# Kernel optimization log

Hardware: AMD Instinct MI355X
Metric: run time of the kernel (lower is better)

## Reference

```python
import jax, jax.numpy as jnp
import numpy as np

N_NODES = 50000
N_EDGES = 800000
N_FEAT = 128
N_HIDDEN = 128
N_CLASSES = 64


def sage_mean_conv(x, src, dst, W_self, W_neigh, b, n_nodes):
    # DGL SAGEConv (mean): out = x @ W_self + mean_neigh(x) @ W_neigh + b
    # mean over in-neighbors: messages flow src -> dst
    msg = x[src]  # [E, F] gather
    h_sum = jax.ops.segment_sum(msg, dst, num_segments=n_nodes)  # [N, F]
    deg = jax.ops.segment_sum(jnp.ones((src.shape[0],), x.dtype), dst,
                              num_segments=n_nodes)
    h_mean = h_sum / jnp.maximum(deg, 1.0)[:, None]
    return x @ W_self + h_mean @ W_neigh + b


def setup_inputs() -> dict:
    key = jax.random.key(0)
    ks = jax.random.split(key, 8)
    sc1 = 1.0 / np.sqrt(N_FEAT)
    sc2 = 1.0 / np.sqrt(N_HIDDEN)
    return {
        "x": jax.random.normal(ks[0], (N_NODES, N_FEAT), jnp.float32),
        "W_self1": jax.random.normal(ks[1], (N_FEAT, N_HIDDEN), jnp.float32) * sc1,
        "W_neigh1": jax.random.normal(ks[2], (N_FEAT, N_HIDDEN), jnp.float32) * sc1,
        "b1": jnp.zeros((N_HIDDEN,), jnp.float32),
        "W_self2": jax.random.normal(ks[3], (N_HIDDEN, N_CLASSES), jnp.float32) * sc2,
        "W_neigh2": jax.random.normal(ks[4], (N_HIDDEN, N_CLASSES), jnp.float32) * sc2,
        "b2": jnp.zeros((N_CLASSES,), jnp.float32),
        "src": jax.random.randint(ks[5], (N_EDGES,), 0, N_NODES, jnp.int32),
        "dst": jax.random.randint(ks[6], (N_EDGES,), 0, N_NODES, jnp.int32),
    }


def reference(x, W_self1, W_neigh1, b1, W_self2, W_neigh2, b2, src, dst):
    n = x.shape[0]
    h = sage_mean_conv(x, src, dst, W_self1, W_neigh1, b1, n)
    h = jax.nn.relu(h)
    logits = sage_mean_conv(h, src, dst, W_self2, W_neigh2, b2, n)
    return logits
```

## Files before the change

### kernel.cpp

```cpp
#include <hip/hip_runtime.h>

#define N_NODES 50000
#define N_EDGES 800000
#define N_FEAT 128
#define N_HIDDEN 128
#define N_CLASSES 64

#define NBUCK 256
#define BUCK_NODES 196
#define BIN_CHUNK 8192
#define BIN_BLK ((N_EDGES + BIN_CHUNK - 1) / BIN_CHUNK)

#define CAST_BLK 6250
#define PACK1_BLK 16
#define PACK2_BLK 8
#define PREP_BLK (CAST_BLK + BIN_BLK + PACK1_BLK + PACK2_BLK)
#define GEMM1_BLK ((N_NODES + 31) / 32)
#define BG_BLK (BIN_BLK + GEMM1_BLK)

typedef __attribute__((ext_vector_type(8))) short bf16x8;
typedef __attribute__((ext_vector_type(4))) float f32x4;

__device__ __forceinline__ unsigned short f32_to_bf16(float f) {
    unsigned int u = __float_as_uint(f);
    return (unsigned short)((u + 0x7fffu + ((u >> 16) & 1u)) >> 16);
}
__device__ __forceinline__ float bf16lo(unsigned int v) { return __uint_as_float(v << 16); }
__device__ __forceinline__ float bf16hi(unsigned int v) { return __uint_as_float(v & 0xffff0000u); }

template <int NOUT>
__device__ void pack_w_body(int idx, const float* __restrict__ Wself,
                            const float* __restrict__ Wneigh,
                            unsigned short* __restrict__ Bp) {
    constexpr int NT = NOUT / 16;
    constexpr int NO = NOUT / 2;
    if (idx >= 4 * NT * 64) return;
    const int lane = idx & 63;
    const int tc = idx >> 6;
    const int c = tc % NT;
    const int t = tc / NT;
    const int n = c * 16 + (lane & 15);
    const int k0 = t * 32 + (lane >> 4) * 8;
    const float* W = (n < NO) ? Wself : Wneigh;
    const int nn = (n < NO) ? n : n - NO;
    ushort4 lo, hi;
    lo.x = f32_to_bf16(W[(k0 + 0) * NO + nn]);
    lo.y = f32_to_bf16(W[(k0 + 1) * NO + nn]);
    lo.z = f32_to_bf16(W[(k0 + 2) * NO + nn]);
    lo.w = f32_to_bf16(W[(k0 + 3) * NO + nn]);
    hi.x = f32_to_bf16(W[(k0 + 4) * NO + nn]);
    hi.y = f32_to_bf16(W[(k0 + 5) * NO + nn]);
    hi.z = f32_to_bf16(W[(k0 + 6) * NO + nn]);
    hi.w = f32_to_bf16(W[(k0 + 7) * NO + nn]);
    ((ushort4*)&Bp[(size_t)idx * 8])[0] = lo;
    ((ushort4*)&Bp[(size_t)idx * 8])[1] = hi;
}

__device__ void a0_body(int blk, const int* __restrict__ dst, int* __restrict__ bcount) {
    __shared__ int h[NBUCK];
    const int t = threadIdx.x;
    h[t] = 0;
    __syncthreads();
    const int lo = blk * BIN_CHUNK;
    const int hi = min(lo + BIN_CHUNK, N_EDGES);
    for (int i = lo + t; i < hi; i += 256) {
        atomicAdd(&h[dst[i] / BUCK_NODES], 1);
    }
    __syncthreads();
    if (h[t] > 0) atomicAdd(&bcount[t], h[t]);
}

__global__ __launch_bounds__(256) void prep_kernel(
        const float* __restrict__ x, unsigned short* __restrict__ xb,
        const int* __restrict__ dst, int* __restrict__ bcount,
        const float* __restrict__ Ws1, const float* __restrict__ Wn1,
        unsigned short* __restrict__ Bp1,
        const float* __restrict__ Ws2, const float* __restrict__ Wn2,
        unsigned short* __restrict__ Bp2) {
    const int b = blockIdx.x;
    const int t = threadIdx.x;
    if (b < CAST_BLK) {
        int i = b * 256 + t;
        float4 v = ((const float4*)x)[i];
        ushort4 o;
        o.x = f32_to_bf16(v.x);
        o.y = f32_to_bf16(v.y);
        o.z = f32_to_bf16(v.z);
        o.w = f32_to_bf16(v.w);
        ((ushort4*)xb)[i] = o;
    } else if (b < CAST_BLK + BIN_BLK) {
        a0_body(b - CAST_BLK, dst, bcount);
    } else if (b < CAST_BLK + BIN_BLK + PACK1_BLK) {
        int idx = (b - CAST_BLK - BIN_BLK) * 256 + t;
        pack_w_body<256>(idx, Ws1, Wn1, Bp1);
    } else {
        int idx = (b - CAST_BLK - BIN_BLK - PACK1_BLK) * 256 + t;
        pack_w_body<128>(idx, Ws2, Wn2, Bp2);
    }
}

__global__ __launch_bounds__(256) void bscan_kernel(const int* __restrict__ bcount,
                                                    int* __restrict__ bstart,
                                                    int* __restrict__ bcursor) {
    __shared__ int sc[NBUCK];
    const int t = threadIdx.x;
    const int v = bcount[t];
    sc[t] = v;
    __syncthreads();
    for (int s = 1; s < NBUCK; s <<= 1) {
        int u = (t >= s) ? sc[t - s] : 0;
        __syncthreads();
        sc[t] += u;
        __syncthreads();
    }
    const int excl = sc[t] - v;
    bstart[t] = excl;
    bcursor[t] = excl;
    if (t == NBUCK - 1) bstart[NBUCK] = sc[t];
}

__device__ void a1_body(int blk, const int* __restrict__ src, const int* __restrict__ dst,
                        int* __restrict__ bcursor, unsigned int* __restrict__ binned) {
    __shared__ int h[NBUCK];
    __shared__ int base[NBUCK];
    const int t = threadIdx.x;
    h[t] = 0;
    __syncthreads();
    const int lo = blk * BIN_CHUNK;
    const int hi = min(lo + BIN_CHUNK, N_EDGES);
    for (int i = lo + t; i < hi; i += 256) {
        atomicAdd(&h[dst[i] / BUCK_NODES], 1);
    }
    __syncthreads();
    if (h[t] > 0) base[t] = atomicAdd(&bcursor[t], h[t]);
    h[t] = 0;
    __syncthreads();
    for (int i = lo + t; i < hi; i += 256) {
        const int d = dst[i];
        const int b = d / BUCK_NODES;
        const int r = atomicAdd(&h[b], 1);
        binned[base[b] + r] = ((unsigned int)(d - b * BUCK_NODES) << 16) | (unsigned int)src[i];
    }
}

template <int NOUT>
__device__ void gemm_mfma_body(int gblk,
                               const unsigned short* __restrict__ xb,
                               const unsigned short* __restrict__ Bp,
                               const float* __restrict__ bias,
                               float* __restrict__ s,
                               unsigned short* __restrict__ p) {
    constexpr int NT = NOUT / 16;
    constexpr int NO = NOUT / 2;
    constexpr int NSUB = NT / 4;

    const int tid = threadIdx.x;
    const int wave = tid >> 6;
    const int lane = tid & 63;
    const int mcol = lane & 15;
    const int kgrp = lane >> 4;

    const int mbase = gblk * 32;
    int r0 = mbase + mcol;       if (r0 >= N_NODES) r0 = N_NODES - 1;
    int r1 = mbase + 16 + mcol;  if (r1 >= N_NODES) r1 = N_NODES - 1;

    f32x4 acc[2][NSUB];
#pragma unroll
    for (int mt = 0; mt < 2; ++mt)
#pragma unroll
        for (int c = 0; c < NSUB; ++c)
            acc[mt][c] = (f32x4){0.f, 0.f, 0.f, 0.f};

#pragma unroll
    for (int t = 0; t < 4; ++t) {
        bf16x8 a0 = *(const bf16x8*)&xb[(size_t)r0 * 128 + t * 32 + kgrp * 8];
        bf16x8 a1 = *(const bf16x8*)&xb[(size_t)r1 * 128 + t * 32 + kgrp * 8];
#pragma unroll
        for (int c = 0; c < NSUB; ++c) {
            const int ct = wave * NSUB + c;
            bf16x8 bfrag = *(const bf16x8*)&Bp[((size_t)(t * NT + ct) * 64 + lane) * 8];
            acc[0][c] = __builtin_amdgcn_mfma_f32_16x16x32_bf16(a0, bfrag, acc[0][c], 0, 0, 0);
            acc[1][c] = __builtin_amdgcn_mfma_f32_16x16x32_bf16(a1, bfrag, acc[1][c], 0, 0, 0);
        }
    }

    float bv[NSUB];
    int ncols[NSUB];
#pragma unroll
    for (int c = 0; c < NSUB; ++c) {
        ncols[c] = (wave * NSUB + c) * 16 + mcol;
        bv[c] = (ncols[c] < NO) ? bias[ncols[c]] : 0.f;
    }

#pragma unroll
    for (int mt = 0; mt < 2; ++mt) {
#pragma unroll
        for (int c = 0; c < NSUB; ++c) {
            const int ncol = ncols[c];
#pragma unroll
            for (int r = 0; r < 4; ++r) {
                const int node = mbase + mt * 16 + kgrp * 4 + r;
                if (node >= N_NODES) continue;
                const float v = acc[mt][c][r];
                if (ncol < NO) {
                    s[(size_t)node * NO + ncol] = v + bv[c];
                } else {
                    p[(size_t)node * NO + (ncol - NO)] = f32_to_bf16(v);
                }
            }
        }
    }
}

__global__ __launch_bounds__(256) void bin_gemm1_kernel(
        const int* __restrict__ src, const int* __restrict__ dst,
        int* __restrict__ bcursor, unsigned int* __restrict__ binned,
        const unsigned short* __restrict__ xb,
        const unsigned short* __restrict__ Bp1,
        const float* __restrict__ b1,
        float* __restrict__ s1, unsigned short* __restrict__ p1) {
    const int b = blockIdx.x;
    if (b < BIN_BLK) {
        a1_body(b, src, dst, bcursor, binned);
    } else {
        gemm_mfma_body<256>(b - BIN_BLK, xb, Bp1, b1, s1, p1);
    }
}

__global__ __launch_bounds__(256) void bucket_build_kernel(
        const unsigned int* __restrict__ binned,
        const int* __restrict__ bstart,
        int* __restrict__ offsets,
        unsigned short* __restrict__ csr16) {
    __shared__ int cnt[NBUCK];
    __shared__ int pre[NBUCK];
    const int b = blockIdx.x;
    const int t = threadIdx.x;
    const int n0 = b * BUCK_NODES;
    const int nn = min(N_NODES - n0, BUCK_NODES);
    const int e0 = bstart[b];
    const int e1 = bstart[b + 1];

    cnt[t] = 0;
    __syncthreads();
    for (int i = e0 + t; i < e1; i += 256) {
        atomicAdd(&cnt[binned[i] >> 16], 1);
    }
    __syncthreads();
    int v = cnt[t];
    pre[t] = v;
    __syncthreads();
    for (int s = 1; s < NBUCK; s <<= 1) {
        int u = (t >= s) ? pre[t - s] : 0;
        __syncthreads();
        pre[t] += u;
        __syncthreads();
    }
    const int excl = pre[t] - v;
    if (t < nn) offsets[n0 + t] = e0 + excl;
    if (b == 0 && t == 0) offsets[N_NODES] = N_EDGES;
    __syncthreads();
    pre[t] = excl;
    cnt[t] = 0;
    __syncthreads();
    for (int i = e0 + t; i < e1; i += 256) {
        const unsigned int u = binned[i];
        const int dl = (int)(u >> 16);
        const int r = atomicAdd(&cnt[dl], 1);
        csr16[e0 + pre[dl] + r] = (unsigned short)(u & 0xffffu);
    }
}

__global__ __launch_bounds__(256) void gemm2_kernel(
        const unsigned short* __restrict__ h1b,
        const unsigned short* __restrict__ Bp2,
        const float* __restrict__ b2,
        float* __restrict__ s2, unsigned short* __restrict__ p2) {
    gemm_mfma_body<128>(blockIdx.x, h1b, Bp2, b2, s2, p2);
}

__global__ __launch_bounds__(256) void agg_relu_128_kernel(
        const float* __restrict__ s,
        const unsigned short* __restrict__ p,
        const int* __restrict__ offsets,
        const unsigned short* __restrict__ csr16,
        unsigned short* __restrict__ h1b) {
    const int wave = threadIdx.x >> 6;
    const int lane = threadIdx.x & 63;
    const int half = lane >> 5;
    const int l = lane & 31;
    const int node = blockIdx.x * 4 + wave;
    if (node >= N_NODES) return;

    const int off0 = offsets[node];
    const int off1 = offsets[node + 1];
    const uint2* pp = (const uint2*)p;

    float a0 = 0.f, a1 = 0.f, a2 = 0.f, a3 = 0.f;
    int i = off0 + half;
    for (; i + 14 < off1; i += 16) {
        uint2 v0 = pp[(size_t)csr16[i + 0] * 32 + l];
        uint2 v1 = pp[(size_t)csr16[i + 2] * 32 + l];
        uint2 v2 = pp[(size_t)csr16[i + 4] * 32 + l];
        uint2 v3 = pp[(size_t)csr16[i + 6] * 32 + l];
        uint2 v4 = pp[(size_t)csr16[i + 8] * 32 + l];
        uint2 v5 = pp[(size_t)csr16[i + 10] * 32 + l];
        uint2 v6 = pp[(size_t)csr16[i + 12] * 32 + l];
        uint2 v7 = pp[(size_t)csr16[i + 14] * 32 + l];
        a0 += bf16lo(v0.x) + bf16lo(v1.x) + bf16lo(v2.x) + bf16lo(v3.x)
            + bf16lo(v4.x) + bf16lo(v5.x) + bf16lo(v6.x) + bf16lo(v7.x);
        a1 += bf16hi(v0.x) + bf16hi(v1.x) + bf16hi(v2.x) + bf16hi(v3.x)
            + bf16hi(v4.x) + bf16hi(v5.x) + bf16hi(v6.x) + bf16hi(v7.x);
        a2 += bf16lo(v0.y) + bf16lo(v1.y) + bf16lo(v2.y) + bf16lo(v3.y)
            + bf16lo(v4.y) + bf16lo(v5.y) + bf16lo(v6.y) + bf16lo(v7.y);
        a3 += bf16hi(v0.y) + bf16hi(v1.y) + bf16hi(v2.y) + bf16hi(v3.y)
            + bf16hi(v4.y) + bf16hi(v5.y) + bf16hi(v6.y) + bf16hi(v7.y);
    }
    for (; i < off1; i += 2) {
        uint2 v = pp[(size_t)csr16[i] * 32 + l];
        a0 += bf16lo(v.x);
        a1 += bf16hi(v.x);
        a2 += bf16lo(v.y);
        a3 += bf16hi(v.y);
    }
    a0 += __shfl_xor(a0, 32);
    a1 += __shfl_xor(a1, 32);
    a2 += __shfl_xor(a2, 32);
    a3 += __shfl_xor(a3, 32);

    if (half == 0) {
        const float invdeg = 1.0f / fmaxf((float)(off1 - off0), 1.0f);
        float4 sv = ((const float4*)s)[(size_t)node * 32 + l];
        ushort4 o;
        o.x = f32_to_bf16(fmaxf(sv.x + a0 * invdeg, 0.f));
        o.y = f32_to_bf16(fmaxf(sv.y + a1 * invdeg, 0.f));
        o.z = f32_to_bf16(fmaxf(sv.z + a2 * invdeg, 0.f));
        o.w = f32_to_bf16(fmaxf(sv.w + a3 * invdeg, 0.f));
        ((ushort4*)h1b)[(size_t)node * 32 + l] = o;
    }
}

__global__ __launch_bounds__(256) void agg_64_kernel(
        const unsigned short* __restrict__ p,
        const int* __restrict__ offsets,
        const unsigned short* __restrict__ csr16,
        float* __restrict__ out) {
    const int wave = threadIdx.x >> 6;
    const int lane = threadIdx.x & 63;
    const int q = lane >> 4;
    const int l = lane & 15;
    const int node = blockIdx.x * 4 + wave;
    if (node >= N_NODES) return;

    const int off0 = offsets[node];
    const int off1 = offsets[node + 1];
    const uint2* pp = (const uint2*)p;

    float a0 = 0.f, a1 = 0.f, a2 = 0.f, a3 = 0.f;
    int i = off0 + q;
    for (; i + 12 < off1; i += 16) {
        uint2 v0 = pp[(size_t)csr16[i + 0] * 16 + l];
        uint2 v1 = pp[(size_t)csr16[i + 4] * 16 + l];
        uint2 v2 = pp[(size_t)csr16[i + 8] * 16 + l];
        uint2 v3 = pp[(size_t)csr16[i + 12] * 16 + l];
        a0 += bf16lo(v0.x) + bf16lo(v1.x) + bf16lo(v2.x) + bf16lo(v3.x);
        a1 += bf16hi(v0.x) + bf16hi(v1.x) + bf16hi(v2.x) + bf16hi(v3.x);
        a2 += bf16lo(v0.y) + bf16lo(v1.y) + bf16lo(v2.y) + bf16lo(v3.y);
        a3 += bf16hi(v0.y) + bf16hi(v1.y) + bf16hi(v2.y) + bf16hi(v3.y);
    }
    for (; i < off1; i += 4) {
        uint2 v = pp[(size_t)csr16[i] * 16 + l];
        a0 += bf16lo(v.x);
        a1 += bf16hi(v.x);
        a2 += bf16lo(v.y);
        a3 += bf16hi(v.y);
    }
    a0 += __shfl_xor(a0, 16); a0 += __shfl_xor(a0, 32);
    a1 += __shfl_xor(a1, 16); a1 += __shfl_xor(a1, 32);
    a2 += __shfl_xor(a2, 16); a2 += __shfl_xor(a2, 32);
    a3 += __shfl_xor(a3, 16); a3 += __shfl_xor(a3, 32);

    if (q == 0) {
        const float invdeg = 1.0f / fmaxf((float)(off1 - off0), 1.0f);
        float4 sv = ((float4*)out)[(size_t)node * 16 + l];
        sv.x += a0 * invdeg;
        sv.y += a1 * invdeg;
        sv.z += a2 * invdeg;
        sv.w += a3 * invdeg;
        ((float4*)out)[(size_t)node * 16 + l] = sv;
    }
}

extern "C" void kernel_launch(void* const* d_in, const int* in_sizes, int n_in,
                              void* d_out, int out_size, void* d_ws, size_t ws_size,
                              hipStream_t stream) {
    const float* x        = (const float*)d_in[0];
    const float* W_self1  = (const float*)d_in[1];
    const float* W_neigh1 = (const float*)d_in[2];
    const float* b1       = (const float*)d_in[3];
    const float* W_self2  = (const float*)d_in[4];
    const float* W_neigh2 = (const float*)d_in[5];
    const float* b2       = (const float*)d_in[6];
    const int*   src      = (const int*)d_in[7];
    const int*   dst      = (const int*)d_in[8];
    float* out = (float*)d_out;

    int* bcount  = (int*)d_ws;
    int* bstart  = bcount + 256;
    int* bcursor = bstart + 288;
    int* offsets = bcursor + 256;
    unsigned int* binned = (unsigned int*)(offsets + 50048);
    unsigned short* csr16 = (unsigned short*)(binned + 800000);
    unsigned short* Bp1 = csr16 + 800000;
    unsigned short* Bp2 = Bp1 + 32768;
    unsigned short* xb  = Bp2 + 16384;
    unsigned short* h1b = xb;
    float* s1 = (float*)(xb + (size_t)N_NODES * 128);
    unsigned short* p1 = (unsigned short*)(s1 + (size_t)N_NODES * 128);
    unsigned short* p2 = p1;

    hipMemsetAsync(bcount, 0, 256 * sizeof(int), stream);
    prep_kernel<<<PREP_BLK, 256, 0, stream>>>(x, xb, dst, bcount,
                                              W_self1, W_neigh1, Bp1,
                                              W_self2, W_neigh2, Bp2);

    bscan_kernel<<<1, 256, 0, stream>>>(bcount, bstart, bcursor);

    bin_gemm1_kernel<<<BG_BLK, 256, 0, stream>>>(src, dst, bcursor, binned,
                                                 xb, Bp1, b1, s1, p1);

    bucket_build_kernel<<<NBUCK, 256, 0, stream>>>(binned, bstart, offsets, csr16);

    agg_relu_128_kernel<<<(N_NODES + 3) / 4, 256, 0, stream>>>(s1, p1, offsets, csr16, h1b);

    gemm2_kernel<<<(N_NODES + 31) / 32, 256, 0, stream>>>(h1b, Bp2, b2, out, p2);
    agg_64_kernel<<<(N_NODES + 3) / 4, 256, 0, stream>>>(p2, offsets, csr16, out);
}
```

Before: 232.0 us.

## Store layer-1 neighbor projections in FP8, reuse per-chunk histograms, widen gather loads

Layer-1 neighbor projections are now stored as FP8 instead of bf16, which halves the bytes moved by the random gather in the first aggregation. Both aggregation kernels are restructured to issue 8 or 4 independent masked wide gathers per iteration, giving more loads in flight. The binning pass now stores per-chunk histograms, so the second pass reuses them instead of recounting, and the memset and global bucket-count atomics are dropped. FP8 storage loses precision in the layer-1 neighbor term and may exceed the accuracy tolerance.

```diff
diff --git a/kernel.cpp b/kernel.cpp
--- a/kernel.cpp
+++ b/kernel.cpp
@@ -1,4 +1,5 @@
 #include <hip/hip_runtime.h>
+#include <hip/hip_fp16.h>
 
 #define N_NODES 50000
 #define N_EDGES 800000
@@ -8,7 +9,7 @@
 
 #define NBUCK 256
 #define BUCK_NODES 196
-#define BIN_CHUNK 8192
+#define BIN_CHUNK 2048
 #define BIN_BLK ((N_EDGES + BIN_CHUNK - 1) / BIN_CHUNK)
 
 #define CAST_BLK 6250
@@ -20,6 +21,7 @@
 
 typedef __attribute__((ext_vector_type(8))) short bf16x8;
 typedef __attribute__((ext_vector_type(4))) float f32x4;
+typedef __attribute__((ext_vector_type(2))) float f32x2;
 
 __device__ __forceinline__ unsigned short f32_to_bf16(float f) {
     unsigned int u = __float_as_uint(f);
@@ -27,6 +29,34 @@
 }
 __device__ __forceinline__ float bf16lo(unsigned int v) { return __uint_as_float(v << 16); }
 __device__ __forceinline__ float bf16hi(unsigned int v) { return __uint_as_float(v & 0xffff0000u); }
+
+#if defined(__has_builtin)
+#if __has_builtin(__builtin_amdgcn_cvt_pk_f32_fp8) && __has_builtin(__builtin_amdgcn_cvt_pk_fp8_f32)
+#define FP8_HW 1
+#endif
+#endif
+
+__device__ __forceinline__ unsigned char f32_to_fp8(float f) {
+#ifdef FP8_HW
+    return (unsigned char)(__builtin_amdgcn_cvt_pk_fp8_f32(f, f, 0, false) & 0xff);
+#else
+    unsigned short hb = __half_as_ushort(__float2half(f));
+    return (unsigned char)((hb + 0x7fu + ((hb >> 8) & 1u)) >> 8);
+#endif
+}
+
+__device__ __forceinline__ void fp8x4_to_f32(unsigned int u, float* o) {
+#ifdef FP8_HW
+    f32x2 lo = __builtin_amdgcn_cvt_pk_f32_fp8(u, false);
+    f32x2 hi = __builtin_amdgcn_cvt_pk_f32_fp8(u, true);
+    o[0] = lo.x; o[1] = lo.y; o[2] = hi.x; o[3] = hi.y;
+#else
+    o[0] = __half2float(__ushort_as_half((unsigned short)((u & 0xffu) << 8)));
+    o[1] = __half2float(__ushort_as_half((unsigned short)(((u >> 8) & 0xffu) << 8)));
+    o[2] = __half2float(__ushort_as_half((unsigned short)(((u >> 16) & 0xffu) << 8)));
+    o[3] = __half2float(__ushort_as_half((unsigned short)(((u >> 24) & 0xffu) << 8)));
+#endif
+}
 
 template <int NOUT>
 __device__ void pack_w_body(int idx, const float* __restrict__ Wself,
@@ -56,7 +86,7 @@
     ((ushort4*)&Bp[(size_t)idx * 8])[1] = hi;
 }
 
-__device__ void a0_body(int blk, const int* __restrict__ dst, int* __restrict__ bcount) {
+__device__ void a0_body(int blk, const int* __restrict__ dst, int* __restrict__ hists) {
     __shared__ int h[NBUCK];
     const int t = threadIdx.x;
     h[t] = 0;
@@ -67,12 +97,12 @@
         atomicAdd(&h[dst[i] / BUCK_NODES], 1);
     }
     __syncthreads();
-    if (h[t] > 0) atomicAdd(&bcount[t], h[t]);
+    hists[blk * NBUCK + t] = h[t];
 }
 
 __global__ __launch_bounds__(256) void prep_kernel(
         const float* __restrict__ x, unsigned short* __restrict__ xb,
-        const int* __restrict__ dst, int* __restrict__ bcount,
+        const int* __restrict__ dst, int* __restrict__ hists,
         const float* __restrict__ Ws1, const float* __restrict__ Wn1,
         unsigned short* __restrict__ Bp1,
         const float* __restrict__ Ws2, const float* __restrict__ Wn2,
@@ -89,7 +119,7 @@
         o.w = f32_to_bf16(v.w);
         ((ushort4*)xb)[i] = o;
     } else if (b < CAST_BLK + BIN_BLK) {
-        a0_body(b - CAST_BLK, dst, bcount);
+        a0_body(b - CAST_BLK, dst, hists);
     } else if (b < CAST_BLK + BIN_BLK + PACK1_BLK) {
         int idx = (b - CAST_BLK - BIN_BLK) * 256 + t;
         pack_w_body<256>(idx, Ws1, Wn1, Bp1);
@@ -99,12 +129,14 @@
     }
 }
 
-__global__ __launch_bounds__(256) void bscan_kernel(const int* __restrict__ bcount,
+__global__ __launch_bounds__(256) void bscan_kernel(const int* __restrict__ hists,
                                                     int* __restrict__ bstart,
                                                     int* __restrict__ bcursor) {
     __shared__ int sc[NBUCK];
     const int t = threadIdx.x;
-    const int v = bcount[t];
+    int v = 0;
+#pragma unroll 8
+    for (int c = 0; c < BIN_BLK; ++c) v += hists[c * NBUCK + t];
     sc[t] = v;
     __syncthreads();
     for (int s = 1; s < NBUCK; s <<= 1) {
@@ -120,36 +152,33 @@
 }
 
 __device__ void a1_body(int blk, const int* __restrict__ src, const int* __restrict__ dst,
+                        const int* __restrict__ hists,
                         int* __restrict__ bcursor, unsigned int* __restrict__ binned) {
-    __shared__ int h[NBUCK];
     __shared__ int base[NBUCK];
+    __shared__ int cnt[NBUCK];
     const int t = threadIdx.x;
-    h[t] = 0;
+    const int h = hists[blk * NBUCK + t];
+    base[t] = atomicAdd(&bcursor[t], h);
+    cnt[t] = 0;
     __syncthreads();
     const int lo = blk * BIN_CHUNK;
     const int hi = min(lo + BIN_CHUNK, N_EDGES);
     for (int i = lo + t; i < hi; i += 256) {
-        atomicAdd(&h[dst[i] / BUCK_NODES], 1);
-    }
-    __syncthreads();
-    if (h[t] > 0) base[t] = atomicAdd(&bcursor[t], h[t]);
-    h[t] = 0;
-    __syncthreads();
-    for (int i = lo + t; i < hi; i += 256) {
         const int d = dst[i];
         const int b = d / BUCK_NODES;
-        const int r = atomicAdd(&h[b], 1);
+        const int r = atomicAdd(&cnt[b], 1);
         binned[base[b] + r] = ((unsigned int)(d - b * BUCK_NODES) << 16) | (unsigned int)src[i];
     }
 }
 
-template <int NOUT>
+template <int NOUT, bool PFP8>
 __device__ void gemm_mfma_body(int gblk,
                                const unsigned short* __restrict__ xb,
                                const unsigned short* __restrict__ Bp,
                                const float* __restrict__ bias,
                                float* __restrict__ s,
-                               unsigned short* __restrict__ p) {
+                               unsigned char* __restrict__ p8,
+                               unsigned short* __restrict__ p16) {
     constexpr int NT = NOUT / 16;
     constexpr int NO = NOUT / 2;
     constexpr int NSUB = NT / 4;
@@ -204,8 +233,10 @@
                 const float v = acc[mt][c][r];
                 if (ncol < NO) {
                     s[(size_t)node * NO + ncol] = v + bv[c];
+                } else if (PFP8) {
+                    p8[(size_t)node * NO + (ncol - NO)] = f32_to_fp8(v);
                 } else {
-                    p[(size_t)node * NO + (ncol - NO)] = f32_to_bf16(v);
+                    p16[(size_t)node * NO + (ncol - NO)] = f32_to_bf16(v);
                 }
             }
         }
@@ -214,16 +245,17 @@
 
 __global__ __launch_bounds__(256) void bin_gemm1_kernel(
         const int* __restrict__ src, const int* __restrict__ dst,
+        const int* __restrict__ hists,
         int* __restrict__ bcursor, unsigned int* __restrict__ binned,
         const unsigned short* __restrict__ xb,
         const unsigned short* __restrict__ Bp1,
         const float* __restrict__ b1,
-        float* __restrict__ s1, unsigned short* __restrict__ p1) {
+        float* __restrict__ s1, unsigned char* __restrict__ p1) {
     const int b = blockIdx.x;
     if (b < BIN_BLK) {
-        a1_body(b, src, dst, bcursor, binned);
+        a1_body(b, src, dst, hists, bcursor, binned);
     } else {
-        gemm_mfma_body<256>(b - BIN_BLK, xb, Bp1, b1, s1, p1);
+        gemm_mfma_body<256, true>(b - BIN_BLK, xb, Bp1, b1, s1, p1, nullptr);
     }
 }
 
@@ -276,19 +308,19 @@
         const unsigned short* __restrict__ Bp2,
         const float* __restrict__ b2,
         float* __restrict__ s2, unsigned short* __restrict__ p2) {
-    gemm_mfma_body<128>(blockIdx.x, h1b, Bp2, b2, s2, p2);
+    gemm_mfma_body<128, false>(blockIdx.x, h1b, Bp2, b2, s2, nullptr, p2);
 }
 
 __global__ __launch_bounds__(256) void agg_relu_128_kernel(
         const float* __restrict__ s,
-        const unsigned short* __restrict__ p,
+        const unsigned char* __restrict__ p,
         const int* __restrict__ offsets,
         const unsigned short* __restrict__ csr16,
         unsigned short* __restrict__ h1b) {
     const int wave = threadIdx.x >> 6;
     const int lane = threadIdx.x & 63;
-    const int half = lane >> 5;
-    const int l = lane & 31;
+    const int q = lane >> 4;
+    const int l = lane & 15;
     const int node = blockIdx.x * 4 + wave;
     if (node >= N_NODES) return;
 
@@ -296,47 +328,55 @@
     const int off1 = offsets[node + 1];
     const uint2* pp = (const uint2*)p;
 
-    float a0 = 0.f, a1 = 0.f, a2 = 0.f, a3 = 0.f;
-    int i = off0 + half;
-    for (; i + 14 < off1; i += 16) {
-        uint2 v0 = pp[(size_t)csr16[i + 0] * 32 + l];
-        uint2 v1 = pp[(size_t)csr16[i + 2] * 32 + l];
-        uint2 v2 = pp[(size_t)csr16[i + 4] * 32 + l];
-        uint2 v3 = pp[(size_t)csr16[i + 6] * 32 + l];
-        uint2 v4 = pp[(size_t)csr16[i + 8] * 32 + l];
-        uint2 v5 = pp[(size_t)csr16[i + 10] * 32 + l];
-        uint2 v6 = pp[(size_t)csr16[i + 12] * 32 + l];
-        uint2 v7 = pp[(size_t)csr16[i + 14] * 32 + l];
-        a0 += bf16lo(v0.x) + bf16lo(v1.x) + bf16lo(v2.x) + bf16lo(v3.x)
-            + bf16lo(v4.x) + bf16lo(v5.x) + bf16lo(v6.x) + bf16lo(v7.x);
-        a1 += bf16hi(v0.x) + bf16hi(v1.x) + bf16hi(v2.x) + bf16hi(v3.x)
-            + bf16hi(v4.x) + bf16hi(v5.x) + bf16hi(v6.x) + bf16hi(v7.x);
-        a2 += bf16lo(v0.y) + bf16lo(v1.y) + bf16lo(v2.y) + bf16lo(v3.y)
-            + bf16lo(v4.y) + bf16lo(v5.y) + bf16lo(v6.y) + bf16lo(v7.y);
-        a3 += bf16hi(v0.y) + bf16hi(v1.y) + bf16hi(v2.y) + bf16hi(v3.y)
-            + bf16hi(v4.y) + bf16hi(v5.y) + bf16hi(v6.y) + bf16hi(v7.y);
-    }
-    for (; i < off1; i += 2) {
-        uint2 v = pp[(size_t)csr16[i] * 32 + l];
-        a0 += bf16lo(v.x);
-        a1 += bf16hi(v.x);
-        a2 += bf16lo(v.y);
-        a3 += bf16hi(v.y);
-    }
-    a0 += __shfl_xor(a0, 32);
-    a1 += __shfl_xor(a1, 32);
-    a2 += __shfl_xor(a2, 32);
-    a3 += __shfl_xor(a3, 32);
-
-    if (half == 0) {
+    float a[8];
+#pragma unroll
+    for (int k = 0; k < 8; ++k) a[k] = 0.f;
+
+    for (int i = off0 + q; i < off1; i += 32) {
+        int idx[8];
+        float m[8];
+        uint2 w[8];
+#pragma unroll
+        for (int j = 0; j < 8; ++j) {
+            const int e = i + 4 * j;
+            const int ec = min(e, off1 - 1);
+            idx[j] = (int)csr16[ec];
+            m[j] = (e < off1) ? 1.f : 0.f;
+        }
+#pragma unroll
+        for (int j = 0; j < 8; ++j) w[j] = pp[(size_t)idx[j] * 16 + l];
+#pragma unroll
+        for (int j = 0; j < 8; ++j) {
+            float d0[4], d1[4];
+            fp8x4_to_f32(w[j].x, d0);
+            fp8x4_to_f32(w[j].y, d1);
+            a[0] += m[j] * d0[0]; a[1] += m[j] * d0[1];
+            a[2] += m[j] * d0[2]; a[3] += m[j] * d0[3];
+            a[4] += m[j] * d1[0]; a[5] += m[j] * d1[1];
+            a[6] += m[j] * d1[2]; a[7] += m[j] * d1[3];
+        }
+    }
+#pragma unroll
+    for (int k = 0; k < 8; ++k) {
+        a[k] += __shfl_xor(a[k], 16);
+        a[k] += __shfl_xor(a[k], 32);
+    }
+
+    if (q == 0) {
         const float invdeg = 1.0f / fmaxf((float)(off1 - off0), 1.0f);
-        float4 sv = ((const float4*)s)[(size_t)node * 32 + l];
-        ushort4 o;
-        o.x = f32_to_bf16(fmaxf(sv.x + a0 * invdeg, 0.f));
-        o.y = f32_to_bf16(fmaxf(sv.y + a1 * invdeg, 0.f));
-        o.z = f32_to_bf16(fmaxf(sv.z + a2 * invdeg, 0.f));
-        o.w = f32_to_bf16(fmaxf(sv.w + a3 * invdeg, 0.f));
-        ((ushort4*)h1b)[(size_t)node * 32 + l] = o;
+        float4 s0 = ((const float4*)s)[(size_t)node * 32 + l * 2];
+        float4 s1 = ((const float4*)s)[(size_t)node * 32 + l * 2 + 1];
+        ushort4 o0, o1;
+        o0.x = f32_to_bf16(fmaxf(s0.x + a[0] * invdeg, 0.f));
+        o0.y = f32_to_bf16(fmaxf(s0.y + a[1] * invdeg, 0.f));
+        o0.z = f32_to_bf16(fmaxf(s0.z + a[2] * invdeg, 0.f));
+        o0.w = f32_to_bf16(fmaxf(s0.w + a[3] * invdeg, 0.f));
+        o1.x = f32_to_bf16(fmaxf(s1.x + a[4] * invdeg, 0.f));
+        o1.y = f32_to_bf16(fmaxf(s1.y + a[5] * invdeg, 0.f));
+        o1.z = f32_to_bf16(fmaxf(s1.z + a[6] * invdeg, 0.f));
+        o1.w = f32_to_bf16(fmaxf(s1.w + a[7] * invdeg, 0.f));
+        ((ushort4*)h1b)[(size_t)node * 32 + l * 2] = o0;
+        ((ushort4*)h1b)[(size_t)node * 32 + l * 2 + 1] = o1;
     }
 }
 
@@ -347,47 +387,57 @@
         float* __restrict__ out) {
     const int wave = threadIdx.x >> 6;
     const int lane = threadIdx.x & 63;
-    const int q = lane >> 4;
-    const int l = lane & 15;
+    const int st = lane >> 3;
+    const int l = lane & 7;
     const int node = blockIdx.x * 4 + wave;
     if (node >= N_NODES) return;
 
     const int off0 = offsets[node];
     const int off1 = offsets[node + 1];
-    const uint2* pp = (const uint2*)p;
-
-    float a0 = 0.f, a1 = 0.f, a2 = 0.f, a3 = 0.f;
-    int i = off0 + q;
-    for (; i + 12 < off1; i += 16) {
-        uint2 v0 = pp[(size_t)csr16[i + 0] * 16 + l];
-        uint2 v1 = pp[(size_t)csr16[i + 4] * 16 + l];
-        uint2 v2 = pp[(size_t)csr16[i + 8] * 16 + l];
-        uint2 v3 = pp[(size_t)csr16[i + 12] * 16 + l];
-        a0 += bf16lo(v0.x) + bf16lo(v1.x) + bf16lo(v2.x) + bf16lo(v3.x);
-        a1 += bf16hi(v0.x) + bf16hi(v1.x) + bf16hi(v2.x) + bf16hi(v3.x);
-        a2 += bf16lo(v0.y) + bf16lo(v1.y) + bf16lo(v2.y) + bf16lo(v3.y);
-        a3 += bf16hi(v0.y) + bf16hi(v1.y) + bf16hi(v2.y) + bf16hi(v3.y);
-    }
-    for (; i < off1; i += 4) {
-        uint2 v = pp[(size_t)csr16[i] * 16 + l];
-        a0 += bf16lo(v.x);
-        a1 += bf16hi(v.x);
-        a2 += bf16lo(v.y);
-        a3 += bf16hi(v.y);
-    }
-    a0 += __shfl_xor(a0, 16); a0 += __shfl_xor(a0, 32);
-    a1 += __shfl_xor(a1, 16); a1 += __shfl_xor(a1, 32);
-    a2 += __shfl_xor(a2, 16); a2 += __shfl_xor(a2, 32);
-    a3 += __shfl_xor(a3, 16); a3 += __shfl_xor(a3, 32);
-
-    if (q == 0) {
+    const uint4* pp = (const uint4*)p;
+
+    float a[8];
+#pragma unroll
+    for (int k = 0; k < 8; ++k) a[k] = 0.f;
+
+    for (int i = off0 + st; i < off1; i += 32) {
+        int idx[4];
+        float m[4];
+        uint4 w[4];
+#pragma unroll
+        for (int j = 0; j < 4; ++j) {
+            const int e = i + 8 * j;
+            const int ec = min(e, off1 - 1);
+            idx[j] = (int)csr16[ec];
+            m[j] = (e < off1) ? 1.f : 0.f;
+        }
+#pragma unroll
+        for (int j = 0; j < 4; ++j) w[j] = pp[(size_t)idx[j] * 8 + l];
+#pragma unroll
+        for (int j = 0; j < 4; ++j) {
+            a[0] += m[j] * bf16lo(w[j].x); a[1] += m[j] * bf16hi(w[j].x);
+            a[2] += m[j] * bf16lo(w[j].y); a[3] += m[j] * bf16hi(w[j].y);
+            a[4] += m[j] * bf16lo(w[j].z); a[5] += m[j] * bf16hi(w[j].z);
+            a[6] += m[j] * bf16lo(w[j].w); a[7] += m[j] * bf16hi(w[j].w);
+        }
+    }
+#pragma unroll
+    for (int k = 0; k < 8; ++k) {
+        a[k] += __shfl_xor(a[k], 8);
+        a[k] += __shfl_xor(a[k], 16);
+        a[k] += __shfl_xor(a[k], 32);
+    }
+
+    if (st == 0) {
         const float invdeg = 1.0f / fmaxf((float)(off1 - off0), 1.0f);
-        float4 sv = ((float4*)out)[(size_t)node * 16 + l];
-        sv.x += a0 * invdeg;
-        sv.y += a1 * invdeg;
-        sv.z += a2 * invdeg;
-        sv.w += a3 * invdeg;
-        ((float4*)out)[(size_t)node * 16 + l] = sv;
+        float4 s0 = ((float4*)out)[(size_t)node * 16 + l * 2];
+        float4 s1 = ((float4*)out)[(size_t)node * 16 + l * 2 + 1];
+        s0.x += a[0] * invdeg; s0.y += a[1] * invdeg;
+        s0.z += a[2] * invdeg; s0.w += a[3] * invdeg;
+        s1.x += a[4] * invdeg; s1.y += a[5] * invdeg;
+        s1.z += a[6] * invdeg; s1.w += a[7] * invdeg;
+        ((float4*)out)[(size_t)node * 16 + l * 2] = s0;
+        ((float4*)out)[(size_t)node * 16 + l * 2 + 1] = s1;
     }
 }
 
@@ -405,34 +455,28 @@
     const int*   dst      = (const int*)d_in[8];
     float* out = (float*)d_out;
 
-    int* bcount  = (int*)d_ws;
-    int* bstart  = bcount + 256;
+    int* bstart  = (int*)d_ws;
     int* bcursor = bstart + 288;
     int* offsets = bcursor + 256;
-    unsigned int* binned = (unsigned int*)(offsets + 50048);
+    int* hists   = offsets + 50048;
+    unsigned int* binned = (unsigned int*)(hists + BIN_BLK * NBUCK);
     unsigned short* csr16 = (unsigned short*)(binned + 800000);
     unsigned short* Bp1 = csr16 + 800000;
     unsigned short* Bp2 = Bp1 + 32768;
     unsigned short* xb  = Bp2 + 16384;
     unsigned short* h1b = xb;
     float* s1 = (float*)(xb + (size_t)N_NODES * 128);
-    unsigned short* p1 = (unsigned short*)(s1 + (size_t)N_NODES * 128);
-    unsigned short* p2 = p1;
-
-    hipMemsetAsync(bcount, 0, 256 * sizeof(int), stream);
-    prep_kernel<<<PREP_BLK, 256, 0, stream>>>(x, xb, dst, bcount,
+    unsigned char* p1 = (unsigned char*)(s1 + (size_t)N_NODES * 128);
+    unsigned short* p2 = (unsigned short*)p1;
+
+    prep_kernel<<<PREP_BLK, 256, 0, stream>>>(x, xb, dst, hists,
                                               W_self1, W_neigh1, Bp1,
                                               W_self2, W_neigh2, Bp2);
-
-    bscan_kernel<<<1, 256, 0, stream>>>(bcount, bstart, bcursor);
-
-    bin_gemm1_kernel<<<BG_BLK, 256, 0, stream>>>(src, dst, bcursor, binned,
+    bscan_kernel<<<1, 256, 0, stream>>>(hists, bstart, bcursor);
+    bin_gemm1_kernel<<<BG_BLK, 256, 0, stream>>>(src, dst, hists, bcursor, binned,
                                                  xb, Bp1, b1, s1, p1);
-
     bucket_build_kernel<<<NBUCK, 256, 0, stream>>>(binned, bstart, offsets, csr16);
-
     agg_relu_128_kernel<<<(N_NODES + 3) / 4, 256, 0, stream>>>(s1, p1, offsets, csr16, h1b);
-
     gemm2_kernel<<<(N_NODES + 31) / 32, 256, 0, stream>>>(h1b, Bp2, b2, out, p2);
     agg_64_kernel<<<(N_NODES + 3) / 4, 256, 0, stream>>>(p2, offsets, csr16, out);
 }
```

Result: faster. 207.8 us (-10.4%).
